# Optimization experiments

Measured on AMD Instinct MI355X. Metric: run time of the kernel, lower is better.

The kernel has to match this reference:

```python
import jax, jax.numpy as jnp
import numpy as np

N_NODES = 50000
N_EDGES = 800000
IN_DIM = 128
HID_DIM = 128
OUT_DIM = 64


def setup_inputs() -> dict:
    key = jax.random.key(0)
    ks = jax.random.split(key, 6)
    x = jax.random.normal(ks[0], (N_NODES, IN_DIM), dtype=jnp.float32)
    edge_index = jax.random.randint(ks[1], (2, N_EDGES), 0, N_NODES, dtype=jnp.int64)
    # per-hop linear weights (torch Linear layout: [out, in], no bias)
    s = 1.0 / np.sqrt(IN_DIM)
    W0 = jax.random.uniform(ks[2], (HID_DIM, IN_DIM), jnp.float32, -s, s)
    W1 = jax.random.uniform(ks[3], (HID_DIM, IN_DIM), jnp.float32, -s, s)
    W2 = jax.random.uniform(ks[4], (HID_DIM, IN_DIM), jnp.float32, -s, s)
    s2 = 1.0 / np.sqrt(HID_DIM * 3)
    Wfc = jax.random.uniform(ks[5], (OUT_DIM, HID_DIM * 3), jnp.float32, -s2, s2)
    return {"x": x, "edge_index": edge_index, "W0": W0, "W1": W1, "W2": W2, "Wfc": Wfc}


def reference(x, edge_index, W0, W1, W2, Wfc):
    N = x.shape[0]
    row, col = edge_index[0], edge_index[1]  # source, target (PyG source_to_target flow)
    # symmetric degree normalization based on in-degree (degree(col, N))
    deg = jax.ops.segment_sum(jnp.ones(row.shape[0], dtype=x.dtype), col, num_segments=N)
    deg_inv_sqrt = jnp.where(deg > 0, jax.lax.rsqrt(jnp.where(deg > 0, deg, 1.0)), 0.0)
    norm = deg_inv_sqrt[row] * deg_inv_sqrt[col]  # [E]
    # NOTE: original code propagates the ORIGINAL x each iteration, so hops 1 and 2
    # both see the 1-hop propagation of x. Faithfully reproduced here.
    px = jax.ops.segment_sum(norm[:, None] * x[row], col, num_segments=N)  # [N, IN_DIM]
    # per-hop linear projections, concat over hops p=[0,1,2]
    h = jnp.concatenate([x @ W0.T, px @ W1.T, px @ W2.T], axis=1)  # [N, 3*HID_DIM]
    return h @ Wfc.T  # [N, OUT_DIM]
```

## Files before the change

kernel.cpp:

```cpp
#include <hip/hip_runtime.h>
#include <hip/hip_bf16.h>

#define N_IN  128
#define N_OUT 64
#define CFB    256
#define MAXNBC 200
#define SLACKC 5120
#define CHUNK  3072
#define PADR   136

typedef __attribute__((ext_vector_type(8))) short short8;
typedef __attribute__((ext_vector_type(4))) float floatx4;
typedef __attribute__((ext_vector_type(2))) float floatx2;

__device__ __forceinline__ unsigned pack_bf16(float a, float b) {
    __hip_bfloat16 ba = __float2bfloat16(a);
    __hip_bfloat16 bb = __float2bfloat16(b);
    unsigned short ua = *(unsigned short*)&ba;
    unsigned short ub = *(unsigned short*)&bb;
    return ((unsigned)ub << 16) | ua;
}
__device__ __forceinline__ float bf16_to_f32(unsigned short u) {
    unsigned v = ((unsigned)u) << 16;
    return *(float*)&v;
}

__global__ __launch_bounds__(256) void prep_kernel(const float* __restrict__ W0,
                                                   const float* __restrict__ W1,
                                                   const float* __restrict__ W2,
                                                   const float* __restrict__ Wfc,
                                                   __hip_bfloat16* __restrict__ CT,
                                                   int* __restrict__ gcur,
                                                   int NBC) {
    if (blockIdx.x == 0) {
        for (int i = threadIdx.x; i < NBC; i += 256) gcur[i] = 0;
    }
    int t = blockIdx.x * 256 + threadIdx.x;
    int n = t >> 7;
    int i = t & 127;
    float a = 0.f;
    if (n < 64) {
        #pragma unroll 4
        for (int k = 0; k < 128; ++k)
            a += Wfc[n * 384 + k] * W0[k * N_IN + i];
    } else {
        int o = n - 64;
        #pragma unroll 4
        for (int k = 0; k < 128; ++k)
            a += Wfc[o * 384 + 128 + k] * W1[k * N_IN + i]
               + Wfc[o * 384 + 256 + k] * W2[k * N_IN + i];
    }
    CT[t] = __float2bfloat16(a);
}

__global__ __launch_bounds__(256) void fillgemm_kernel(
        const int* __restrict__ ei,
        int* __restrict__ gcur,
        unsigned* __restrict__ gsorted,
        const float* __restrict__ x,
        const __hip_bfloat16* __restrict__ CT,
        float* __restrict__ out,
        __hip_bfloat16* __restrict__ z16,
        int E, int N, int NFB) {
    __shared__ __align__(16) char smem[(64 + 128) * PADR * 2];
    int tid = threadIdx.x;
    int bid = blockIdx.x;

    if (bid < NFB) {
        int* lcnt = (int*)smem;
        int* gbase_s = lcnt + MAXNBC;
        int base = bid * CHUNK;
        for (int i = tid; i < MAXNBC; i += 256) lcnt[i] = 0;
        __syncthreads();
        int myc[CHUNK / 256];
        #pragma unroll
        for (int q = 0; q < CHUNK / 256; ++q) {
            int e = base + q * 256 + tid;
            int c = (e < E) ? ei[E + e] : -1;
            myc[q] = c;
            if (c >= 0) atomicAdd(&lcnt[c >> 8], 1);
        }
        __syncthreads();
        for (int f = tid; f < MAXNBC; f += 256) {
            int n = lcnt[f];
            gbase_s[f] = (n > 0) ? (f * SLACKC + atomicAdd(&gcur[f], n)) : 0;
        }
        __syncthreads();
        #pragma unroll
        for (int q = 0; q < CHUNK / 256; ++q) {
            int c = myc[q];
            if (c >= 0) {
                int e = base + q * 256 + tid;
                unsigned r = (unsigned)ei[e];
                int p = atomicAdd(&gbase_s[c >> 8], 1);
                if (p < ((c >> 8) + 1) * SLACKC)
                    gsorted[p] = ((unsigned)c << 16) | r;
            }
        }
        return;
    }

    unsigned short* xs = (unsigned short*)smem;
    unsigned short* Bs = xs + 64 * PADR;
    int base = (bid - NFB) * 64;

    {
        int row = tid >> 2;
        int colq = (tid & 3) * 32;
        int node = base + row;
        unsigned tmp[16];
        if (node < N) {
            const float4* src = (const float4*)(x + (size_t)node * N_IN + colq);
            #pragma unroll
            for (int q = 0; q < 8; ++q) {
                float4 v = src[q];
                tmp[q * 2]     = pack_bf16(v.x, v.y);
                tmp[q * 2 + 1] = pack_bf16(v.z, v.w);
            }
        } else {
            #pragma unroll
            for (int q = 0; q < 16; ++q) tmp[q] = 0u;
        }
        unsigned* dst = (unsigned*)(xs + row * PADR + colq);
        #pragma unroll
        for (int q = 0; q < 16; ++q) dst[q] = tmp[q];
    }
    {
        const unsigned* src = (const unsigned*)CT;
        for (int c = tid; c < 8192; c += 256) {
            int row = c >> 6;
            int col = (c & 63) * 2;
            *(unsigned*)(Bs + row * PADR + col) = src[c];
        }
    }
    __syncthreads();

    int wave = tid >> 6, lane = tid & 63;
    int wm = wave & 1, wn = wave >> 1;
    int quad = lane >> 4, l16 = lane & 15;

    floatx4 acc[2][4];
    #pragma unroll
    for (int mt = 0; mt < 2; ++mt)
        #pragma unroll
        for (int nt = 0; nt < 4; ++nt)
            acc[mt][nt] = (floatx4){0.f, 0.f, 0.f, 0.f};

    #pragma unroll
    for (int kc = 0; kc < 4; ++kc) {
        int kof = kc * 32 + quad * 8;
        short8 afr[2], bfr[4];
        #pragma unroll
        for (int mt = 0; mt < 2; ++mt)
            afr[mt] = *(const short8*)(xs + (wm * 32 + mt * 16 + l16) * PADR + kof);
        #pragma unroll
        for (int nt = 0; nt < 4; ++nt)
            bfr[nt] = *(const short8*)(Bs + (wn * 64 + nt * 16 + l16) * PADR + kof);
        #pragma unroll
        for (int mt = 0; mt < 2; ++mt)
            #pragma unroll
            for (int nt = 0; nt < 4; ++nt)
                acc[mt][nt] = __builtin_amdgcn_mfma_f32_16x16x32_bf16(
                    afr[mt], bfr[nt], acc[mt][nt], 0, 0, 0);
    }

    #pragma unroll
    for (int mt = 0; mt < 2; ++mt) {
        #pragma unroll
        for (int reg = 0; reg < 4; ++reg) {
            int node = base + wm * 32 + mt * 16 + quad * 4 + reg;
            if (node >= N) continue;
            if (wn == 0) {
                #pragma unroll
                for (int nt = 0; nt < 4; ++nt)
                    out[(size_t)node * N_OUT + nt * 16 + l16] = acc[mt][nt][reg];
            } else {
                #pragma unroll
                for (int nt = 0; nt < 4; ++nt)
                    z16[((size_t)node << 6) + nt * 16 + l16] =
                        __float2bfloat16(acc[mt][nt][reg]);
            }
        }
    }
}

__global__ __launch_bounds__(256) void sort_kernel(
        const int* __restrict__ gcur,
        const unsigned* __restrict__ gsorted,
        unsigned short* __restrict__ srow,
        int* __restrict__ offs,
        int* __restrict__ cnt,
        float* __restrict__ dis,
        int N) {
    __shared__ __align__(16) char smem[SLACKC * 4 + 3 * 256 * 4];
    int tid = threadIdx.x;
    unsigned* ev = (unsigned*)smem;
    int* c256 = (int*)(smem + SLACKC * 4);
    int* cur  = c256 + 256;
    int* ts   = cur + 256;
    int f = blockIdx.x;
    int lo = f * SLACKC;
    int m = min(gcur[f], SLACKC);
    for (int i = tid; i < m; i += 256) ev[i] = gsorted[lo + i];
    c256[tid] = 0;
    __syncthreads();
    for (int i = tid; i < m; i += 256)
        atomicAdd(&c256[(ev[i] >> 16) & (CFB - 1)], 1);
    __syncthreads();
    int v = c256[tid];
    int xx = v;
    ts[tid] = xx;
    __syncthreads();
    for (int off = 1; off < 256; off <<= 1) {
        int t2 = (tid >= off) ? ts[tid - off] : 0;
        __syncthreads();
        xx += t2; ts[tid] = xx;
        __syncthreads();
    }
    int b = xx - v;
    cur[tid] = b;
    int node = f * CFB + tid;
    if (node < N) {
        offs[node] = lo + b;
        cnt[node] = v;
        dis[node] = v > 0 ? rsqrtf((float)v) : 0.f;
    }
    __syncthreads();
    for (int i = tid; i < m; i += 256) {
        unsigned val = ev[i];
        int cl = (val >> 16) & (CFB - 1);
        int p = atomicAdd(&cur[cl], 1);
        srow[lo + p] = (unsigned short)(val & 0xffffu);
    }
}

__global__ __launch_bounds__(256) void scale_kernel(
        const __hip_bfloat16* __restrict__ z16,
        const float* __restrict__ dis,
        unsigned char* __restrict__ z8,
        int N) {
    int t = blockIdx.x * 256 + threadIdx.x;
    if (t >= N * 8) return;
    int node = t >> 3;
    float d = dis[node];
    short8 v = *(const short8*)((const unsigned short*)z16 + (size_t)t * 8);
    float f[8];
    #pragma unroll
    for (int j = 0; j < 8; ++j)
        f[j] = bf16_to_f32((unsigned short)v[j]) * d;
    unsigned lo = 0, hi = 0;
    lo = __builtin_amdgcn_cvt_pk_fp8_f32(f[0], f[1], lo, false);
    lo = __builtin_amdgcn_cvt_pk_fp8_f32(f[2], f[3], lo, true);
    hi = __builtin_amdgcn_cvt_pk_fp8_f32(f[4], f[5], hi, false);
    hi = __builtin_amdgcn_cvt_pk_fp8_f32(f[6], f[7], hi, true);
    uint2 o; o.x = lo; o.y = hi;
    *(uint2*)(z8 + (size_t)t * 8) = o;
}

__global__ __launch_bounds__(256) void gather_kernel(
        const int* __restrict__ offs, const int* __restrict__ cnt,
        const unsigned short* __restrict__ srow, const unsigned char* __restrict__ z8,
        float* __restrict__ out, int N) {
    int lane = threadIdx.x & 63;
    int quarter = lane >> 4;
    int ql   = lane & 15;
    int sub  = ql >> 3;
    int jj   = ql & 7;
    int node = blockIdx.x * 16 + (threadIdx.x >> 6) * 4 + quarter;
    int start = 0, deg = 0;
    if (node < N) { start = offs[node]; deg = cnt[node]; }
    floatx2 a2[4];
    #pragma unroll
    for (int q = 0; q < 4; ++q) a2[q] = (floatx2){0.f, 0.f};
    for (int k0 = 0; k0 < deg; k0 += 16) {
        int m = min(16, deg - k0);
        int idx = 0;
        if (ql < m)
            idx = (int)srow[start + k0 + ql];
        #pragma unroll
        for (int it = 0; it < 8; ++it) {
            int s0 = it * 2 + sub;
            int src0 = (lane & 48) | s0;
            int r0 = __shfl(idx, src0);
            uint2 u0 = make_uint2(0u, 0u);
            if (s0 < m) u0 = *(const uint2*)(z8 + ((size_t)r0 << 6) + jj * 8);
            a2[0] += __builtin_amdgcn_cvt_pk_f32_fp8(u0.x, false);
            a2[1] += __builtin_amdgcn_cvt_pk_f32_fp8(u0.x, true);
            a2[2] += __builtin_amdgcn_cvt_pk_f32_fp8(u0.y, false);
            a2[3] += __builtin_amdgcn_cvt_pk_f32_fp8(u0.y, true);
        }
    }
    #pragma unroll
    for (int q = 0; q < 4; ++q) {
        a2[q].x += __shfl_xor(a2[q].x, 8);
        a2[q].y += __shfl_xor(a2[q].y, 8);
    }
    if (ql < 8 && deg > 0) {
        float dn = rsqrtf((float)deg);
        float4* op = (float4*)(out + ((size_t)node << 6) + jj * 8);
        float4 o0 = op[0], o1 = op[1];
        o0.x += dn * a2[0].x; o0.y += dn * a2[0].y;
        o0.z += dn * a2[1].x; o0.w += dn * a2[1].y;
        o1.x += dn * a2[2].x; o1.y += dn * a2[2].y;
        o1.z += dn * a2[3].x; o1.w += dn * a2[3].y;
        op[0] = o0; op[1] = o1;
    }
}

extern "C" void kernel_launch(void* const* d_in, const int* in_sizes, int n_in,
                              void* d_out, int out_size, void* d_ws, size_t ws_size,
                              hipStream_t stream) {
    const float* x   = (const float*)d_in[0];
    const int*   ei  = (const int*)d_in[1];
    const float* W0  = (const float*)d_in[2];
    const float* W1  = (const float*)d_in[3];
    const float* W2  = (const float*)d_in[4];
    const float* Wfc = (const float*)d_in[5];
    float* out = (float*)d_out;
    int N = in_sizes[0] / N_IN;
    int E = in_sizes[1] / 2;
    int NBC = (N + CFB - 1) / CFB;
    int GB  = (N + 63) / 64;
    int NFB = (E + CHUNK - 1) / CHUNK;

    __hip_bfloat16* CT = (__hip_bfloat16*)d_ws;
    int*   cnt     = (int*)((char*)d_ws + 32768);
    float* dis     = (float*)(cnt + N);
    int*   gcur    = (int*)(dis + N);
    int*   offs    = gcur + NBC;
    unsigned* gsorted = (unsigned*)(offs + N);
    unsigned short* srow = (unsigned short*)(gsorted + (size_t)NBC * SLACKC);
    size_t zoff = ((size_t)((char*)(srow + (size_t)NBC * SLACKC) - (char*)d_ws) + 63)
                  & ~(size_t)63;
    unsigned char* z8 = (unsigned char*)d_ws + zoff;
    size_t z16off = (zoff + (size_t)N * 64 + 63) & ~(size_t)63;
    __hip_bfloat16* z16 = (__hip_bfloat16*)((char*)d_ws + z16off);

    prep_kernel<<<64, 256, 0, stream>>>(W0, W1, W2, Wfc, CT, gcur, NBC);
    fillgemm_kernel<<<NFB + GB, 256, 0, stream>>>(ei, gcur, gsorted, x, CT,
                                                  out, z16, E, N, NFB);
    sort_kernel<<<NBC, 256, 0, stream>>>(gcur, gsorted, srow, offs, cnt, dis, N);
    scale_kernel<<<(N * 8 + 255) / 256, 256, 0, stream>>>(z16, dis, z8, N);
    gather_kernel<<<(N + 15) / 16, 256, 0, stream>>>(offs, cnt, srow, z8, out, N);
}
```

Before: 131.7 us.

## Fuse fp8 scaling into sort kernel and widen gather loads to 16 bytes

The separate scale kernel is removed. Each sort-block thread now scales and converts its own node's 64-element bf16 row to fp8, using the in-degree it has just computed, so the dis array and one launch go away. The gather kernel now has each lane load 16 bytes of fp8 per neighbor instead of 8, with 4 neighbor slots per pass and an extra shuffle reduction. The fused scale step uses only 196 blocks with per-thread strided row access, which may coalesce worse than the old dedicated kernel.

```diff
diff --git a/kernel.cpp b/kernel.cpp
--- a/kernel.cpp
+++ b/kernel.cpp
@@ -184,13 +184,14 @@
     }
 }
 
-__global__ __launch_bounds__(256) void sort_kernel(
+__global__ __launch_bounds__(256) void sortscale_kernel(
         const int* __restrict__ gcur,
         const unsigned* __restrict__ gsorted,
         unsigned short* __restrict__ srow,
         int* __restrict__ offs,
         int* __restrict__ cnt,
-        float* __restrict__ dis,
+        const __hip_bfloat16* __restrict__ z16,
+        unsigned char* __restrict__ z8,
         int N) {
     __shared__ __align__(16) char smem[SLACKC * 4 + 3 * 256 * 4];
     int tid = threadIdx.x;
@@ -223,7 +224,6 @@
     if (node < N) {
         offs[node] = lo + b;
         cnt[node] = v;
-        dis[node] = v > 0 ? rsqrtf((float)v) : 0.f;
     }
     __syncthreads();
     for (int i = tid; i < m; i += 256) {
@@ -232,29 +232,27 @@
         int p = atomicAdd(&cur[cl], 1);
         srow[lo + p] = (unsigned short)(val & 0xffffu);
     }
-}
-
-__global__ __launch_bounds__(256) void scale_kernel(
-        const __hip_bfloat16* __restrict__ z16,
-        const float* __restrict__ dis,
-        unsigned char* __restrict__ z8,
-        int N) {
-    int t = blockIdx.x * 256 + threadIdx.x;
-    if (t >= N * 8) return;
-    int node = t >> 3;
-    float d = dis[node];
-    short8 v = *(const short8*)((const unsigned short*)z16 + (size_t)t * 8);
-    float f[8];
-    #pragma unroll
-    for (int j = 0; j < 8; ++j)
-        f[j] = bf16_to_f32((unsigned short)v[j]) * d;
-    unsigned lo = 0, hi = 0;
-    lo = __builtin_amdgcn_cvt_pk_fp8_f32(f[0], f[1], lo, false);
-    lo = __builtin_amdgcn_cvt_pk_fp8_f32(f[2], f[3], lo, true);
-    hi = __builtin_amdgcn_cvt_pk_fp8_f32(f[4], f[5], hi, false);
-    hi = __builtin_amdgcn_cvt_pk_fp8_f32(f[6], f[7], hi, true);
-    uint2 o; o.x = lo; o.y = hi;
-    *(uint2*)(z8 + (size_t)t * 8) = o;
+
+    if (node < N) {
+        float d = (v > 0) ? rsqrtf((float)v) : 0.f;
+        const unsigned short* zr = (const unsigned short*)z16 + ((size_t)node << 6);
+        unsigned char* zw = z8 + ((size_t)node << 6);
+        #pragma unroll
+        for (int h = 0; h < 8; ++h) {
+            short8 vv = *(const short8*)(zr + h * 8);
+            float fb[8];
+            #pragma unroll
+            for (int j = 0; j < 8; ++j)
+                fb[j] = bf16_to_f32((unsigned short)vv[j]) * d;
+            unsigned lo2 = 0, hi2 = 0;
+            lo2 = __builtin_amdgcn_cvt_pk_fp8_f32(fb[0], fb[1], lo2, false);
+            lo2 = __builtin_amdgcn_cvt_pk_fp8_f32(fb[2], fb[3], lo2, true);
+            hi2 = __builtin_amdgcn_cvt_pk_fp8_f32(fb[4], fb[5], hi2, false);
+            hi2 = __builtin_amdgcn_cvt_pk_fp8_f32(fb[6], fb[7], hi2, true);
+            uint2 o; o.x = lo2; o.y = hi2;
+            *(uint2*)(zw + h * 8) = o;
+        }
+    }
 }
 
 __global__ __launch_bounds__(256) void gather_kernel(
@@ -264,46 +262,55 @@
     int lane = threadIdx.x & 63;
     int quarter = lane >> 4;
     int ql   = lane & 15;
-    int sub  = ql >> 3;
-    int jj   = ql & 7;
+    int slot = ql >> 2;
+    int jj   = ql & 3;
     int node = blockIdx.x * 16 + (threadIdx.x >> 6) * 4 + quarter;
     int start = 0, deg = 0;
     if (node < N) { start = offs[node]; deg = cnt[node]; }
-    floatx2 a2[4];
-    #pragma unroll
-    for (int q = 0; q < 4; ++q) a2[q] = (floatx2){0.f, 0.f};
+    floatx2 a2[8];
+    #pragma unroll
+    for (int q = 0; q < 8; ++q) a2[q] = (floatx2){0.f, 0.f};
     for (int k0 = 0; k0 < deg; k0 += 16) {
         int m = min(16, deg - k0);
         int idx = 0;
         if (ql < m)
             idx = (int)srow[start + k0 + ql];
         #pragma unroll
-        for (int it = 0; it < 8; ++it) {
-            int s0 = it * 2 + sub;
+        for (int it = 0; it < 4; ++it) {
+            int s0 = it * 4 + slot;
             int src0 = (lane & 48) | s0;
             int r0 = __shfl(idx, src0);
-            uint2 u0 = make_uint2(0u, 0u);
-            if (s0 < m) u0 = *(const uint2*)(z8 + ((size_t)r0 << 6) + jj * 8);
-            a2[0] += __builtin_amdgcn_cvt_pk_f32_fp8(u0.x, false);
-            a2[1] += __builtin_amdgcn_cvt_pk_f32_fp8(u0.x, true);
-            a2[2] += __builtin_amdgcn_cvt_pk_f32_fp8(u0.y, false);
-            a2[3] += __builtin_amdgcn_cvt_pk_f32_fp8(u0.y, true);
-        }
-    }
-    #pragma unroll
-    for (int q = 0; q < 4; ++q) {
+            uint4 u = make_uint4(0u, 0u, 0u, 0u);
+            if (s0 < m) u = *(const uint4*)(z8 + ((size_t)r0 << 6) + jj * 16);
+            a2[0] += __builtin_amdgcn_cvt_pk_f32_fp8(u.x, false);
+            a2[1] += __builtin_amdgcn_cvt_pk_f32_fp8(u.x, true);
+            a2[2] += __builtin_amdgcn_cvt_pk_f32_fp8(u.y, false);
+            a2[3] += __builtin_amdgcn_cvt_pk_f32_fp8(u.y, true);
+            a2[4] += __builtin_amdgcn_cvt_pk_f32_fp8(u.z, false);
+            a2[5] += __builtin_amdgcn_cvt_pk_f32_fp8(u.z, true);
+            a2[6] += __builtin_amdgcn_cvt_pk_f32_fp8(u.w, false);
+            a2[7] += __builtin_amdgcn_cvt_pk_f32_fp8(u.w, true);
+        }
+    }
+    #pragma unroll
+    for (int q = 0; q < 8; ++q) {
+        a2[q].x += __shfl_xor(a2[q].x, 4);
+        a2[q].y += __shfl_xor(a2[q].y, 4);
         a2[q].x += __shfl_xor(a2[q].x, 8);
         a2[q].y += __shfl_xor(a2[q].y, 8);
     }
-    if (ql < 8 && deg > 0) {
+    if (ql < 4 && deg > 0) {
         float dn = rsqrtf((float)deg);
-        float4* op = (float4*)(out + ((size_t)node << 6) + jj * 8);
-        float4 o0 = op[0], o1 = op[1];
-        o0.x += dn * a2[0].x; o0.y += dn * a2[0].y;
-        o0.z += dn * a2[1].x; o0.w += dn * a2[1].y;
-        o1.x += dn * a2[2].x; o1.y += dn * a2[2].y;
-        o1.z += dn * a2[3].x; o1.w += dn * a2[3].y;
-        op[0] = o0; op[1] = o1;
+        float4* op = (float4*)(out + ((size_t)node << 6) + jj * 16);
+        #pragma unroll
+        for (int k = 0; k < 4; ++k) {
+            float4 o = op[k];
+            o.x += dn * a2[2 * k].x;
+            o.y += dn * a2[2 * k].y;
+            o.z += dn * a2[2 * k + 1].x;
+            o.w += dn * a2[2 * k + 1].y;
+            op[k] = o;
+        }
     }
 }
 
@@ -325,8 +332,7 @@
 
     __hip_bfloat16* CT = (__hip_bfloat16*)d_ws;
     int*   cnt     = (int*)((char*)d_ws + 32768);
-    float* dis     = (float*)(cnt + N);
-    int*   gcur    = (int*)(dis + N);
+    int*   gcur    = cnt + N;
     int*   offs    = gcur + NBC;
     unsigned* gsorted = (unsigned*)(offs + N);
     unsigned short* srow = (unsigned short*)(gsorted + (size_t)NBC * SLACKC);
@@ -339,7 +345,7 @@
     prep_kernel<<<64, 256, 0, stream>>>(W0, W1, W2, Wfc, CT, gcur, NBC);
     fillgemm_kernel<<<NFB + GB, 256, 0, stream>>>(ei, gcur, gsorted, x, CT,
                                                   out, z16, E, N, NFB);
-    sort_kernel<<<NBC, 256, 0, stream>>>(gcur, gsorted, srow, offs, cnt, dis, N);
-    scale_kernel<<<(N * 8 + 255) / 256, 256, 0, stream>>>(z16, dis, z8, N);
+    sortscale_kernel<<<NBC, 256, 0, stream>>>(gcur, gsorted, srow, offs, cnt,
+                                              z16, z8, N);
     gather_kernel<<<(N + 15) / 16, 256, 0, stream>>>(offs, cnt, srow, z8, out, N);
 }
```

Measured after the change: 131.9 us. Within noise of the previous version (+0.2%).
